# Kernel tuning notes

Hardware: AMD Instinct MI355X
Metric: run time of the kernel (lower is better)

The kernel has to match this reference:

```python
import jax, jax.numpy as jnp
import numpy as np

NUM_HEADS = 16
EPS = 1e-6


def rmsnorm(x, w):
    return x * jax.lax.rsqrt(jnp.mean(x * x, axis=-1, keepdims=True) + EPS) * w


def split_heads(x):
    b, t, d = x.shape
    return x.reshape(b, t, NUM_HEADS, d // NUM_HEADS).transpose(0, 2, 1, 3)


def setup_inputs() -> dict:
    key = jax.random.key(0)
    ks = jax.random.split(key, 16)
    B, S, D, F, N = 4, 2048, 1024, 4096, 16

    def xavier(k, shape):
        lim = float(np.sqrt(6.0 / (shape[-2] + shape[-1])))
        return jax.random.uniform(k, shape, jnp.float32, -lim, lim)

    return {
        'sequence_tokens': jax.random.normal(ks[0], (B, S, D), jnp.float32),
        'sequence_mask': jnp.ones((B, S), dtype=bool),
        'ns_tokens': jax.random.normal(ks[1], (B, N, D), jnp.float32),
        'ns_mask': jnp.ones((B, N), dtype=bool),
        'next_sequence_length': 1024,
        'attn_norm_w': jnp.ones((D,), jnp.float32),
        'ffn_norm_w': jnp.ones((D,), jnp.float32),
        'Wq': xavier(ks[2], (D, D)),
        'Wk': xavier(ks[3], (D, D)),
        'Wv': xavier(ks[4], (D, D)),
        'Wo': xavier(ks[5], (D, D)),
        'ns_q_w': xavier(ks[6], (N, D, D)),
        'ns_k_w': xavier(ks[7], (N, D, D)),
        'ns_v_w': xavier(ks[8], (N, D, D)),
        'seq_up_w': xavier(ks[9], (D, F)),
        'seq_up_b': jnp.zeros((F,), jnp.float32),
        'seq_down_w': xavier(ks[10], (F, D)),
        'seq_down_b': jnp.zeros((D,), jnp.float32),
        'ns_up_w': xavier(ks[11], (N, D, F)),
        'ns_up_b': jnp.zeros((N, F), jnp.float32),
        'ns_down_w': xavier(ks[12], (N, F, D)),
        'ns_down_b': jnp.zeros((N, D), jnp.float32),
    }


def reference(sequence_tokens, sequence_mask, ns_tokens, ns_mask, next_sequence_length,
              attn_norm_w, ffn_norm_w, Wq, Wk, Wv, Wo,
              ns_q_w, ns_k_w, ns_v_w,
              seq_up_w, seq_up_b, seq_down_w, seq_down_b,
              ns_up_w, ns_up_b, ns_down_w, ns_down_b):
    nsl = next_sequence_length
    B, S, D = sequence_tokens.shape
    N = ns_tokens.shape[1]
    scale = 1.0 / np.sqrt(D // NUM_HEADS)

    # --- attention block (pre-norm) ---
    x_seq = rmsnorm(sequence_tokens, attn_norm_w)
    x_ns = rmsnorm(ns_tokens, attn_norm_w)
    seq_q_mask = sequence_mask[:, -nsl:]

    q = jnp.concatenate([x_seq[:, -nsl:] @ Wq, jnp.einsum('bnd,ndo->bno', x_ns, ns_q_w)], axis=1)
    k = jnp.concatenate([x_seq @ Wk, jnp.einsum('bnd,ndo->bno', x_ns, ns_k_w)], axis=1)
    v = jnp.concatenate([x_seq @ Wv, jnp.einsum('bnd,ndo->bno', x_ns, ns_v_w)], axis=1)
    q, k, v = split_heads(q), split_heads(k), split_heads(v)

    total_k = S + N
    q_pos = jnp.concatenate([jnp.arange(S - nsl, S), jnp.arange(S, total_k)])
    k_pos = jnp.arange(total_k)
    causal = k_pos[None, :] <= q_pos[:, None]                       # [nsl+N, S+N]
    key_mask = jnp.concatenate([sequence_mask, ns_mask], axis=1)    # [B, S+N]

    logits = jnp.einsum('bhqd,bhkd->bhqk', q.astype(jnp.float32), k.astype(jnp.float32)) * scale
    logits = jnp.where(causal[None, None] & key_mask[:, None, None, :], logits, -10000.0)
    attw = jax.nn.softmax(logits, axis=-1).astype(q.dtype)
    att = jnp.einsum('bhqk,bhkd->bhqd', attw, v)
    att = att.transpose(0, 2, 1, 3).reshape(B, nsl + N, D) @ Wo

    seq_att = att[:, :nsl] * seq_q_mask[..., None].astype(att.dtype)
    ns_att = att[:, nsl:] * ns_mask[..., None].astype(att.dtype)

    seq = sequence_tokens[:, -nsl:] + seq_att
    ns = ns_tokens + ns_att

    # --- FFN block (pre-norm, SiLU) ---
    h_seq = rmsnorm(seq, ffn_norm_w)
    h_ns = rmsnorm(ns, ffn_norm_w)
    seq_ffn = jax.nn.silu(h_seq @ seq_up_w + seq_up_b) @ seq_down_w + seq_down_b
    seq_ffn = seq_ffn * seq_q_mask[..., None].astype(seq_ffn.dtype)
    ns_h = jax.nn.silu(jnp.einsum('bnd,ndf->bnf', h_ns, ns_up_w) + ns_up_b)
    ns_ffn = jnp.einsum('bnf,nfd->bnd', ns_h, ns_down_w) + ns_down_b
    ns_ffn = ns_ffn * ns_mask[..., None].astype(ns_ffn.dtype)

    seq_out = (seq + seq_ffn) * seq_q_mask[..., None].astype(seq.dtype)
    ns_out = (ns + ns_ffn) * ns_mask[..., None].astype(ns.dtype)
    return seq_out, seq_q_mask, ns_out, ns_mask
```

## Files before the change

### kernel.cpp

```cpp
#include <hip/hip_runtime.h>
#include <hip/hip_bf16.h>
#include <cstdint>
#include <cstddef>

#define BB 4
#define SS 2048
#define DD 1024
#define FF 4096
#define NN 16
#define HH 16
#define HD 64
#define NSL 1024
#define TQ 1040
#define TK 2064

typedef __attribute__((ext_vector_type(8))) short short8v;
typedef __attribute__((ext_vector_type(4))) float f32x4;
typedef __attribute__((ext_vector_type(16))) float f32x16;
typedef __hip_bfloat16 bf16;

#define SCLOG2E 0.1803368801111092f

__device__ __forceinline__ void gload16(const bf16* g, bf16* l) {
    __builtin_amdgcn_global_load_lds(
        (const __attribute__((address_space(1))) unsigned int*)(const void*)g,
        (__attribute__((address_space(3))) unsigned int*)(void*)l,
        16, 0, 0);
}

__device__ __forceinline__ unsigned cvtpk(float lo, float hi2) {
    unsigned r;
    asm("v_cvt_pk_bf16_f32 %0, %1, %2" : "=v"(r) : "v"(lo), "v"(hi2));
    return r;
}

__device__ __forceinline__ void convT_body(
    const float* __restrict__ W, bf16* __restrict__ WT, int K, int N,
    int bx, int by, char* smem)
{
    bf16 (*T)[65] = (bf16(*)[65])smem;
    const int tid = threadIdx.x;
    const int c0 = bx * 64;
    const int r0 = by * 64;
    const int rr = tid >> 6, c = tid & 63;
#pragma unroll
    for (int j = 0; j < 16; j++) {
        int row = j * 4 + rr;
        T[row][c] = __float2bfloat16(W[(size_t)(r0 + row) * N + c0 + c]);
    }
    __syncthreads();
#pragma unroll
    for (int j = 0; j < 16; j++) {
        int wrow = j * 4 + rr;
        WT[(size_t)(c0 + wrow) * K + r0 + c] = T[c][wrow];
    }
}

__device__ __forceinline__ void rmsnorm_body(
    const float* __restrict__ x, const float* __restrict__ w,
    bf16* __restrict__ out, int row, char* smem)
{
    float* red = (float*)smem;
    const int tid = threadIdx.x;
    const float* xp = x + (size_t)row * DD + tid * 4;
    float4 xv = *(const float4*)xp;
    float ss = xv.x * xv.x + xv.y * xv.y + xv.z * xv.z + xv.w * xv.w;
#pragma unroll
    for (int o = 32; o >= 1; o >>= 1) ss += __shfl_down(ss, o);
    if ((tid & 63) == 0) red[tid >> 6] = ss;
    __syncthreads();
    float tot = red[0] + red[1] + red[2] + red[3];
    float rs = rsqrtf(tot * (1.0f / DD) + 1e-6f);
    float4 wv = *(const float4*)(w + tid * 4);
    bf16* op = out + (size_t)row * DD + tid * 4;
    op[0] = __float2bfloat16(xv.x * rs * wv.x);
    op[1] = __float2bfloat16(xv.y * rs * wv.y);
    op[2] = __float2bfloat16(xv.z * rs * wv.z);
    op[3] = __float2bfloat16(xv.w * rs * wv.w);
}

__global__ __launch_bounds__(256) void prep_kernel(
    const float* __restrict__ Wq, const float* __restrict__ Wk,
    const float* __restrict__ Wv, const float* __restrict__ Wo,
    const float* __restrict__ upw, const float* __restrict__ dww,
    bf16* __restrict__ wqkvT, bf16* __restrict__ woT,
    bf16* __restrict__ upwT, bf16* __restrict__ dwwT,
    const float* __restrict__ seq_tokens, const float* __restrict__ ns_tokens,
    const float* __restrict__ attn_norm_w,
    bf16* __restrict__ xnseq, bf16* __restrict__ xnns,
    float* __restrict__ resb, float* __restrict__ outz,
    float* __restrict__ nsacc)
{
    __shared__ __align__(16) char smem[8448];
    int id = blockIdx.x;
    if (id < 256)        convT_body(Wq, wqkvT, 1024, 1024, id & 15, id >> 4, smem);
    else if (id < 512)   { int u = id - 256;  convT_body(Wk, wqkvT + 1024 * 1024, 1024, 1024, u & 15, u >> 4, smem); }
    else if (id < 768)   { int u = id - 512;  convT_body(Wv, wqkvT + 2048 * 1024, 1024, 1024, u & 15, u >> 4, smem); }
    else if (id < 1024)  { int u = id - 768;  convT_body(Wo, woT, 1024, 1024, u & 15, u >> 4, smem); }
    else if (id < 2048)  { int u = id - 1024; convT_body(upw, upwT, 1024, 4096, u & 63, u >> 6, smem); }
    else if (id < 3072)  { int u = id - 2048; convT_body(dww, dwwT, 4096, 1024, u & 15, u >> 4, smem); }
    else if (id < 11264) rmsnorm_body(seq_tokens, attn_norm_w, xnseq, id - 3072, smem);
    else if (id < 11328) rmsnorm_body(ns_tokens, attn_norm_w, xnns, id - 11264, smem);
    else {
        int u = id - 11328;
        float* base;
        if (u < 4160)       base = resb + (size_t)u * 1024;
        else if (u < 8256)  base = outz + (size_t)(u - 4160) * 1024;
        else                base = nsacc + (size_t)(u - 8256) * 1024;
        float4 z = {0.f, 0.f, 0.f, 0.f};
        ((float4*)base)[threadIdx.x] = z;
    }
}

__global__ __launch_bounds__(256) void rmsnorm_kernel(
    const float* __restrict__ x, const float* __restrict__ w,
    bf16* __restrict__ out)
{
    __shared__ __align__(16) char smem[64];
    rmsnorm_body(x, w, out, blockIdx.x, smem);
}

template<int EPI>
__device__ __forceinline__ void gemm128_body(
    int bxx, int byy, int bzz, char* smem,
    const bf16* __restrict__ A, const bf16* __restrict__ BT,
    void* __restrict__ Cp, int M, int Nn, int K, int kTot,
    int aMb, int aRS, int aOff,
    const float* __restrict__ bias,
    const float* __restrict__ res0, const float* __restrict__ res1)
{
    const int m0 = bxx * 128;
    const int n0 = byy * 128;
    if constexpr (EPI == 4) {
        if (n0 < 1024 && (m0 & 2047) < 1024) return;
    }
    bf16* As = (bf16*)smem;
    bf16* Bs = (bf16*)(smem + 16384);
    const int tid = threadIdx.x;
    const int lane = tid & 63;
    const int wave = tid >> 6;
    const int wr = (wave >> 1) * 64;
    const int wc = (wave & 1) * 64;
    const int ql = lane & 31;
    const int hi = lane >> 5;
    const int kOff = bzz * K;

    const int srow = tid >> 3;
    const int skc = (((tid & 7) ^ (srow & 7))) * 8;
    const bf16* pA[4];
    const bf16* pB[4];
#pragma unroll
    for (int g = 0; g < 4; g++) {
        int ar = m0 + g * 32 + srow; if (ar >= M) ar = M - 1;
        pA[g] = A + ((size_t)(ar / aMb) * aRS + (ar % aMb) + aOff) * kTot + kOff + skc;
        pB[g] = BT + (size_t)(n0 + g * 32 + srow) * kTot + kOff + skc;
    }
    bf16* lA = As + tid * 8;
    bf16* lB = Bs + tid * 8;

    const int rA0 = wr + ql, rA1 = wr + 32 + ql;
    const int rB0 = wc + ql, rB1 = wc + 32 + ql;

    f32x16 acc[2][2] = {};

    for (int k0 = 0; k0 < K; k0 += 64) {
        __syncthreads();
#pragma unroll
        for (int g = 0; g < 4; g++) {
            gload16(pA[g] + k0, lA + g * 2048);
            gload16(pB[g] + k0, lB + g * 2048);
        }
        __syncthreads();
#pragma unroll
        for (int ks = 0; ks < 4; ks++) {
            int ch = 2 * ks + hi;
            short8v a0 = *(const short8v*)(&As[(rA0 << 6) + ((ch ^ (rA0 & 7)) << 3)]);
            short8v a1 = *(const short8v*)(&As[(rA1 << 6) + ((ch ^ (rA1 & 7)) << 3)]);
            short8v b0 = *(const short8v*)(&Bs[(rB0 << 6) + ((ch ^ (rB0 & 7)) << 3)]);
            short8v b1 = *(const short8v*)(&Bs[(rB1 << 6) + ((ch ^ (rB1 & 7)) << 3)]);
            acc[0][0] = __builtin_amdgcn_mfma_f32_32x32x16_bf16(a0, b0, acc[0][0], 0, 0, 0);
            acc[0][1] = __builtin_amdgcn_mfma_f32_32x32x16_bf16(a0, b1, acc[0][1], 0, 0, 0);
            acc[1][0] = __builtin_amdgcn_mfma_f32_32x32x16_bf16(a1, b0, acc[1][0], 0, 0, 0);
            acc[1][1] = __builtin_amdgcn_mfma_f32_32x32x16_bf16(a1, b1, acc[1][1], 0, 0, 0);
        }
    }

#pragma unroll
    for (int mt = 0; mt < 2; mt++)
#pragma unroll
        for (int nt = 0; nt < 2; nt++) {
            const int colg = n0 + wc + nt * 32 + ql;
#pragma unroll
            for (int g = 0; g < 4; g++) {
                int row0 = m0 + wr + mt * 32 + g * 8 + 4 * hi;
                if constexpr (EPI == 4) {
                    int bb2 = row0 >> 11, s0 = row0 & 2047;
                    if (colg < 1024) {
                        if (s0 >= 1024) {
#pragma unroll
                            for (int j = 0; j < 4; j++)
                                ((bf16*)Cp)[((size_t)(bb2 * TQ + s0 + j - 1024)) * DD + colg] =
                                    __float2bfloat16(acc[mt][nt][g * 4 + j] * SCLOG2E);
                        }
                    } else if (colg < 2048) {
#pragma unroll
                        for (int j = 0; j < 4; j++)
                            ((bf16*)res0)[((size_t)(bb2 * TK + s0 + j)) * DD + (colg - 1024)] =
                                __float2bfloat16(acc[mt][nt][g * 4 + j]);
                    } else {
                        union { unsigned u[2]; } pk_;
                        pk_.u[0] = cvtpk(acc[mt][nt][g * 4 + 0], acc[mt][nt][g * 4 + 1]);
                        pk_.u[1] = cvtpk(acc[mt][nt][g * 4 + 2], acc[mt][nt][g * 4 + 3]);
                        bf16* vt = (bf16*)res1;
                        *(uint2*)(&vt[((size_t)(bb2 * DD + colg - 2048)) * TK + s0]) =
                            *(const uint2*)pk_.u;
                    }
                    continue;
                }
#pragma unroll
                for (int j = 0; j < 4; j++) {
                    int row = row0 + j;
                    if (row >= M) continue;
                    float val = acc[mt][nt][g * 4 + j];
                    if constexpr (EPI == 1) {
                        val += bias[colg];
                        val = val / (1.0f + __expf(-val));
                        ((bf16*)Cp)[(size_t)row * Nn + colg] = __float2bfloat16(val);
                    } else if constexpr (EPI == 5) {
                        float* dst = (float*)Cp + (size_t)row * DD + colg;
                        if (bzz == 0) {
                            int bb2 = row / TQ, t = row % TQ;
                            const float* rp = (t < NSL)
                                ? res0 + ((size_t)bb2 * SS + (SS - NSL) + t) * DD
                                : res1 + ((size_t)bb2 * NN + (t - NSL)) * DD;
                            atomicAdd(dst, val + rp[colg]);
                        } else {
                            atomicAdd(dst, val);
                        }
                    } else if constexpr (EPI == 6) {
                        float* dst = (float*)Cp + (size_t)row * DD + colg;
                        if (bzz == 0) {
                            int bb2 = row / NSL, t = row % NSL;
                            float r = res0[((size_t)bb2 * TQ + t) * DD + colg];
                            atomicAdd(dst, val + bias[colg] + r);
                        } else {
                            atomicAdd(dst, val);
                        }
                    }
                }
            }
        }
}

template<int EPI>
__global__ __launch_bounds__(256, 3) void gemm128_kernel(
    const bf16* __restrict__ A, const bf16* __restrict__ BT,
    void* __restrict__ Cp, int M, int Nn, int K, int kTot,
    int aMb, int aRS, int aOff,
    const float* __restrict__ bias,
    const float* __restrict__ res0, const float* __restrict__ res1)
{
    __shared__ __align__(16) char smem[32768];
    gemm128_body<EPI>(blockIdx.x, blockIdx.y, blockIdx.z, smem,
                      A, BT, Cp, M, Nn, K, kTot, aMb, aRS, aOff,
                      bias, res0, res1);
}

__device__ __forceinline__ void ns_qkv_body(
    int cb, int n, int which, char* smem,
    const bf16* __restrict__ xnns,
    const float* __restrict__ Wqn, const float* __restrict__ Wkn,
    const float* __restrict__ Wvn,
    bf16* __restrict__ q, bf16* __restrict__ k, bf16* __restrict__ vbt)
{
    float* Asm = (float*)smem;
    float* RedF = (float*)(smem + 16384);
    const int tid = threadIdx.x;
    const int cg = tid & 63;
    const int dg = tid >> 6;
    const int col = cb * 64 + cg;
    const float* W = which == 0 ? Wqn : (which == 1 ? Wkn : Wvn);
    for (int i = tid; i < 512; i += 256) {
        int bb = i >> 7, c8 = (i & 127) * 8;
        uint4 raw = *(const uint4*)&xnns[((size_t)(bb * NN + n)) * DD + c8];
        const bf16* hh = (const bf16*)&raw;
#pragma unroll
        for (int j = 0; j < 8; j++) Asm[bb * 1024 + c8 + j] = __bfloat162float(hh[j]);
    }
    __syncthreads();
    float a0 = 0, a1 = 0, a2 = 0, a3 = 0;
    const float* wp = W + (size_t)n * DD * DD + col;
#pragma unroll 8
    for (int d = dg * 256; d < dg * 256 + 256; d++) {
        float w = wp[(size_t)d * DD];
        a0 += Asm[0 * 1024 + d] * w; a1 += Asm[1 * 1024 + d] * w;
        a2 += Asm[2 * 1024 + d] * w; a3 += Asm[3 * 1024 + d] * w;
    }
    RedF[(dg * 4 + 0) * 64 + cg] = a0; RedF[(dg * 4 + 1) * 64 + cg] = a1;
    RedF[(dg * 4 + 2) * 64 + cg] = a2; RedF[(dg * 4 + 3) * 64 + cg] = a3;
    __syncthreads();
    if (dg == 0) {
#pragma unroll
        for (int bb = 0; bb < 4; bb++) {
            float s = RedF[(0 * 4 + bb) * 64 + cg] + RedF[(1 * 4 + bb) * 64 + cg]
                    + RedF[(2 * 4 + bb) * 64 + cg] + RedF[(3 * 4 + bb) * 64 + cg];
            if (which == 0)
                q[((size_t)(bb * TQ + NSL + n)) * DD + col] =
                    __float2bfloat16(s * SCLOG2E);
            else if (which == 1)
                k[((size_t)(bb * TK + SS + n)) * DD + col] = __float2bfloat16(s);
            else
                vbt[((size_t)(bb * DD + col)) * TK + SS + n] = __float2bfloat16(s);
        }
    }
}

__device__ __forceinline__ void ns_up_body(
    int cb, int n, char* smem,
    const bf16* __restrict__ hb, const float* __restrict__ W,
    const float* __restrict__ bias, bf16* __restrict__ mid)
{
    float* Asm = (float*)smem;
    float* RedF = (float*)(smem + 16384);
    const int tid = threadIdx.x;
    const int cg = tid & 63;
    const int dg = tid >> 6;
    const int col = cb * 64 + cg;
    for (int i = tid; i < 512; i += 256) {
        int bb = i >> 7, c8 = (i & 127) * 8;
        uint4 raw = *(const uint4*)&hb[((size_t)(bb * TQ + NSL + n)) * DD + c8];
        const bf16* hh = (const bf16*)&raw;
#pragma unroll
        for (int j = 0; j < 8; j++) Asm[bb * 1024 + c8 + j] = __bfloat162float(hh[j]);
    }
    __syncthreads();
    float a0 = 0, a1 = 0, a2 = 0, a3 = 0;
    const float* wp = W + (size_t)n * DD * FF + col;
#pragma unroll 8
    for (int d = dg * 256; d < dg * 256 + 256; d++) {
        float w = wp[(size_t)d * FF];
        a0 += Asm[0 * 1024 + d] * w; a1 += Asm[1 * 1024 + d] * w;
        a2 += Asm[2 * 1024 + d] * w; a3 += Asm[3 * 1024 + d] * w;
    }
    RedF[(dg * 4 + 0) * 64 + cg] = a0; RedF[(dg * 4 + 1) * 64 + cg] = a1;
    RedF[(dg * 4 + 2) * 64 + cg] = a2; RedF[(dg * 4 + 3) * 64 + cg] = a3;
    __syncthreads();
    if (dg == 0) {
        float bv = bias[(size_t)n * FF + col];
#pragma unroll
        for (int bb = 0; bb < 4; bb++) {
            float x = RedF[(0 * 4 + bb) * 64 + cg] + RedF[(1 * 4 + bb) * 64 + cg]
                    + RedF[(2 * 4 + bb) * 64 + cg] + RedF[(3 * 4 + bb) * 64 + cg] + bv;
            x = x / (1.0f + __expf(-x));
            mid[((size_t)(bb * NN + n)) * FF + col] = __float2bfloat16(x);
        }
    }
}

__device__ __forceinline__ void ns_down_body(
    int cb, int n, int z, char* smem,
    const bf16* __restrict__ mid, const float* __restrict__ W,
    float* __restrict__ accum)
{
    float* Asm = (float*)smem;
    float* RedF = (float*)(smem + 16384);
    const int tid = threadIdx.x;
    const int cg = tid & 63;
    const int dg = tid >> 6;
    const int col = cb * 64 + cg;
    for (int i = tid; i < 512; i += 256) {
        int bb = i >> 7, c8 = (i & 127) * 8;
        uint4 raw = *(const uint4*)&mid[((size_t)(bb * NN + n)) * FF + z * 1024 + c8];
        const bf16* hh = (const bf16*)&raw;
#pragma unroll
        for (int j = 0; j < 8; j++) Asm[bb * 1024 + c8 + j] = __bfloat162float(hh[j]);
    }
    __syncthreads();
    float a0 = 0, a1 = 0, a2 = 0, a3 = 0;
    const float* wp = W + ((size_t)n * FF + z * 1024) * DD + col;
#pragma unroll 8
    for (int d = dg * 256; d < dg * 256 + 256; d++) {
        float w = wp[(size_t)d * DD];
        a0 += Asm[0 * 1024 + d] * w; a1 += Asm[1 * 1024 + d] * w;
        a2 += Asm[2 * 1024 + d] * w; a3 += Asm[3 * 1024 + d] * w;
    }
    RedF[(dg * 4 + 0) * 64 + cg] = a0; RedF[(dg * 4 + 1) * 64 + cg] = a1;
    RedF[(dg * 4 + 2) * 64 + cg] = a2; RedF[(dg * 4 + 3) * 64 + cg] = a3;
    __syncthreads();
    if (dg == 0) {
#pragma unroll
        for (int bb = 0; bb < 4; bb++) {
            float s = RedF[(0 * 4 + bb) * 64 + cg] + RedF[(1 * 4 + bb) * 64 + cg]
                    + RedF[(2 * 4 + bb) * 64 + cg] + RedF[(3 * 4 + bb) * 64 + cg];
            atomicAdd(&accum[((size_t)(bb * NN + n)) * DD + col], s);
        }
    }
}

__global__ __launch_bounds__(256, 3) void fusedA_kernel(
    const bf16* __restrict__ xnseq, const bf16* __restrict__ wqkvT,
    bf16* __restrict__ qb, bf16* __restrict__ kb, bf16* __restrict__ vbt,
    const bf16* __restrict__ xnns,
    const float* __restrict__ Wqn, const float* __restrict__ Wkn,
    const float* __restrict__ Wvn)
{
    __shared__ __align__(16) char smem[32768];
    int flat = blockIdx.x;
    int g = flat / 3, r = flat - g * 3;
    if (r < 2) {
        int gi = g * 2 + r;
        gemm128_body<4>(gi & 63, gi >> 6, 0, smem, xnseq, wqkvT, qb,
            8192, 3072, 1024, 1024, 8192, 8192, 0,
            nullptr, (const float*)kb, (const float*)vbt);
    } else {
        ns_qkv_body(g & 15, (g >> 4) & 15, g >> 8, smem,
                    xnns, Wqn, Wkn, Wvn, qb, kb, vbt);
    }
}

__global__ __launch_bounds__(256, 3) void fusedB_kernel(
    const bf16* __restrict__ hb, const bf16* __restrict__ upwT,
    bf16* __restrict__ midseq, const float* __restrict__ upb,
    const float* __restrict__ nupw, const float* __restrict__ nupb,
    bf16* __restrict__ midns)
{
    __shared__ __align__(16) char smem[32768];
    int flat = blockIdx.x;
    int g = flat >> 1, r = flat & 1;
    if (r == 0) {
        gemm128_body<1>(g & 31, g >> 5, 0, smem, hb, upwT, midseq,
            4096, 4096, 1024, 1024, 1024, 1040, 0,
            upb, nullptr, nullptr);
    } else {
        ns_up_body(g & 63, g >> 6, smem, hb, nupw, nupb, midns);
    }
}

__global__ __launch_bounds__(256, 3) void fusedC_kernel(
    const bf16* __restrict__ midseq, const bf16* __restrict__ dwwT,
    float* __restrict__ out, const float* __restrict__ dwb,
    const float* __restrict__ resb,
    const bf16* __restrict__ midns, const float* __restrict__ ndww,
    float* __restrict__ nsacc)
{
    __shared__ __align__(16) char smem[32768];
    int flat = blockIdx.x;
    int g = flat >> 1, r = flat & 1;
    if (r == 0) {
        gemm128_body<6>(g & 31, (g >> 5) & 7, g >> 8, smem, midseq, dwwT, out,
            4096, 1024, 1024, 4096, 4096, 4096, 0,
            dwb, resb, nullptr);
    } else {
        ns_down_body(g & 15, (g >> 4) & 15, g >> 8, smem, midns, ndww, nsacc);
    }
}

#define SWZ(row, chunk) (((row) << 6) + ((((chunk) ^ ((row) & 7))) << 3))
#define DEFER_THR 12.0f

__global__ __launch_bounds__(128, 3) void attn_mfma_kernel(
    const bf16* __restrict__ qb, const bf16* __restrict__ kb,
    const bf16* __restrict__ vbt, float* __restrict__ pO,
    float* __restrict__ pML)
{
    __shared__ bf16 SM[2 * 8192];

    const int tid = threadIdx.x;
    const int lane = tid & 63;
    const int w = tid >> 6;

    int flat = blockIdx.x + 34 * (blockIdx.y + 16 * blockIdx.z);
    int widx = (flat & 7) * 272 + (flat >> 3);
    const int bx = widx % 34;
    const int rem = widx / 34;
    const int h = rem & 15;
    const int b = rem >> 4;
    const int qt = 16 - (bx >> 1);
    const int kh = bx & 1;

    const int q0 = qt * 64;
    const int ql = lane & 31;
    const int hi = lane >> 5;
    const int qg = q0 + 32 * w + ql;
    const bool wact = (q0 + 32 * w) < TQ;
    const int qpos = NSL + qg;

    short8v qf[4] = {};
    if (qg < TQ) {
        const bf16* qp = qb + ((size_t)(b * TQ + qg)) * DD + h * HD;
#pragma unroll
        for (int s = 0; s < 4; s++) qf[s] = *(const short8v*)(qp + 16 * s + 8 * hi);
    }

    const int qlast = min(q0 + 63, TQ - 1);
    const int nkt = (NSL + qlast + 1 + 63) >> 6;
    const int khmid = nkt >> 1;
    const int k0t = kh ? khmid : 0;
    const int k1t = kh ? nkt : khmid;

    int off[2][4];
#pragma unroll
    for (int t = 0; t < 2; t++)
#pragma unroll
        for (int s = 0; s < 4; s++)
            off[t][s] = SWZ(ql + 32 * t, 2 * s + hi);

    const int c = lane & 7;
    size_t kSrc[4], vRow[4];
    int vSw[4], sRow[4];
#pragma unroll
    for (int i = 0; i < 4; i++) {
        int r = 32 * w + 8 * i + (lane >> 3);
        sRow[i] = r;
        kSrc[i] = ((size_t)(b * TK + r)) * DD + h * HD + ((c ^ (r & 7)) << 3);
        vRow[i] = ((size_t)(b * DD + h * HD + r)) * TK;
        vSw[i]  = (c ^ (r & 7)) << 3;
    }

    auto stage = [&](int kbase, int buf) {
        bf16* kD = SM + buf * 8192 + w * 2048;
        bf16* vD = SM + buf * 8192 + 4096 + w * 2048;
        if (kbase + 64 <= TK) {
#pragma unroll
            for (int i = 0; i < 4; i++) {
                gload16(kb + kSrc[i] + (size_t)kbase * DD, kD + i * 512);
                gload16(vbt + vRow[i] + kbase + vSw[i], vD + i * 512);
            }
        } else {
#pragma unroll
            for (int i = 0; i < 4; i++) {
                int rg = min(kbase + sRow[i], TK - 1);
                gload16(kb + ((size_t)(b * TK + rg)) * DD + h * HD +
                             ((c ^ (sRow[i] & 7)) << 3), kD + i * 512);
                int colv = (kbase + vSw[i] + 8 <= TK) ? (kbase + vSw[i]) : 0;
                gload16(vbt + vRow[i] + colv, vD + i * 512);
            }
        }
    };

    float m_run = -1e30f, l_run = 0.f;
    f32x16 o0 = {}, o1 = {};
    const int wlimit = NSL + q0 + 32 * w + 31;

    int cur = 0;
    stage(k0t * 64, 0);

    for (int kt = k0t; kt < k1t; kt++) {
        const int kbase = kt * 64;
        __syncthreads();
        if (kt + 1 < k1t) stage(kbase + 64, cur ^ 1);

        if (wact && kbase <= wlimit) {
            const bf16* KsC = SM + cur * 8192;
            const bf16* VtC = KsC + 4096;

            f32x16 st[2] = {};
            __builtin_amdgcn_s_setprio(1);
#pragma unroll
            for (int s = 0; s < 4; s++) {
                short8v kf0 = *(const short8v*)(&KsC[off[0][s]]);
                short8v kf1 = *(const short8v*)(&KsC[off[1][s]]);
                st[0] = __builtin_amdgcn_mfma_f32_32x32x16_bf16(kf0, qf[s], st[0], 0, 0, 0);
                st[1] = __builtin_amdgcn_mfma_f32_32x32x16_bf16(kf1, qf[s], st[1], 0, 0, 0);
            }
            __builtin_amdgcn_s_setprio(0);

            if (kbase + 63 > NSL + q0 + 32 * w) {
#pragma unroll
                for (int t = 0; t < 2; t++)
#pragma unroll
                    for (int r = 0; r < 16; r++) {
                        int key = kbase + 32 * t + (r & 3) + 8 * (r >> 2) + 4 * hi;
                        if (key > qpos) st[t][r] = -1e30f;
                    }
            }

            float pmax = st[0][0];
#pragma unroll
            for (int r = 1; r < 16; r++) pmax = fmaxf(pmax, st[0][r]);
#pragma unroll
            for (int r = 0; r < 16; r++) pmax = fmaxf(pmax, st[1][r]);
            pmax = fmaxf(pmax, __shfl_xor(pmax, 32));

            if (!__all(pmax - m_run <= DEFER_THR)) {
                float mnew = fmaxf(m_run, pmax);
                float alpha = exp2f(m_run - mnew);
                m_run = mnew;
                l_run *= alpha;
#pragma unroll
                for (int r = 0; r < 16; r++) {
                    float aq = __shfl(alpha, (r & 3) + 8 * (r >> 2) + 4 * hi);
                    o0[r] *= aq; o1[r] *= aq;
                }
            }

            unsigned nib[8][2];
            float lt = 0.f;
#pragma unroll
            for (int m8 = 0; m8 < 8; m8++) {
                int t = m8 >> 2, rb = (m8 & 3) * 4;
                float p0 = exp2f(st[t][rb + 0] - m_run);
                float p1 = exp2f(st[t][rb + 1] - m_run);
                float p2 = exp2f(st[t][rb + 2] - m_run);
                float p3 = exp2f(st[t][rb + 3] - m_run);
                lt += (p0 + p1) + (p2 + p3);
                nib[m8][0] = cvtpk(p0, p1);
                nib[m8][1] = cvtpk(p2, p3);
            }
            lt += __shfl_xor(lt, 32);
            l_run += lt;

            __builtin_amdgcn_s_setprio(1);
#pragma unroll
            for (int s = 0; s < 4; s++) {
                unsigned s0 = nib[2 * s + 1 - hi][0];
                unsigned s1 = nib[2 * s + 1 - hi][1];
                unsigned r0 = __shfl_xor(s0, 32);
                unsigned r1 = __shfl_xor(s1, 32);
                unsigned w0 = hi ? r0 : nib[2 * s][0];
                unsigned w1 = hi ? r1 : nib[2 * s][1];
                unsigned w2 = hi ? nib[2 * s + 1][0] : r0;
                unsigned w3 = hi ? nib[2 * s + 1][1] : r1;
                union { unsigned u[4]; short8v v; } pa;
                pa.u[0] = w0; pa.u[1] = w1; pa.u[2] = w2; pa.u[3] = w3;
                short8v vf0 = *(const short8v*)(&VtC[off[0][s]]);
                short8v vf1 = *(const short8v*)(&VtC[off[1][s]]);
                o0 = __builtin_amdgcn_mfma_f32_32x32x16_bf16(pa.v, vf0, o0, 0, 0, 0);
                o1 = __builtin_amdgcn_mfma_f32_32x32x16_bf16(pa.v, vf1, o1, 0, 0, 0);
            }
            __builtin_amdgcn_s_setprio(0);
        }
        cur ^= 1;
    }

    if (wact) {
        size_t pb = ((size_t)((b * HH + h) * 17 + qt)) * 2 + kh;
        float* Op = pO + pb * 4096 + (size_t)(32 * w) * 64;
#pragma unroll
        for (int r = 0; r < 16; r++) {
            int qrow = (r & 3) + 8 * (r >> 2) + 4 * hi;
            Op[qrow * 64 + ql]      = o0[r];
            Op[qrow * 64 + 32 + ql] = o1[r];
        }
        if (hi == 0) {
            pML[pb * 128 + 32 * w + ql] = m_run;
            pML[pb * 128 + 64 + 32 * w + ql] = l_run;
        }
    }
}

__global__ __launch_bounds__(256) void attn_merge_kernel(
    const float* __restrict__ pO, const float* __restrict__ pML,
    bf16* __restrict__ atb)
{
    const int qt = 16 - blockIdx.x;
    const int h = blockIdx.y, b = blockIdx.z;
    const int q0 = qt * 64;
    const int tid = threadIdx.x;
    const int q = tid >> 2;
    const int d0 = (tid & 3) * 16;
    if (q0 + q >= TQ) return;
    size_t pb0 = ((size_t)((b * HH + h) * 17 + qt)) * 2;
    float ma = pML[pb0 * 128 + q],       la = pML[pb0 * 128 + 64 + q];
    float mb = pML[(pb0 + 1) * 128 + q], lb = pML[(pb0 + 1) * 128 + 64 + q];
    float m = fmaxf(ma, mb);
    float wa = exp2f(ma - m), wb = exp2f(mb - m);
    float inv = 1.0f / (la * wa + lb * wb);
    const float* Oa = pO + pb0 * 4096 + q * 64 + d0;
    const float* Ob = Oa + 4096;
    union { unsigned u[8]; uint4 q4[2]; } outp;
#pragma unroll
    for (int j = 0; j < 8; j++) {
        float x0 = (Oa[2 * j]     * wa + Ob[2 * j]     * wb) * inv;
        float x1 = (Oa[2 * j + 1] * wa + Ob[2 * j + 1] * wb) * inv;
        outp.u[j] = cvtpk(x0, x1);
    }
    bf16* op = atb + ((size_t)(b * TQ + q0 + q)) * DD + h * HD + d0;
    *(uint4*)op = outp.q4[0];
    *(uint4*)(op + 8) = outp.q4[1];
}

__global__ __launch_bounds__(256) void ns_final_kernel(
    const float* __restrict__ accum, const float* __restrict__ bias,
    const float* __restrict__ res, float* __restrict__ out)
{
    const int blk = blockIdx.x;
    const int tid = threadIdx.x;
    if (blk < 64) {
        const int b = blk >> 4, n = blk & 15;
        float* outns = out + 4198400;
        for (int c = tid; c < DD; c += 256) {
            float x = accum[(size_t)blk * DD + c] + bias[(size_t)n * DD + c]
                    + res[((size_t)(b * TQ + NSL + n)) * DD + c];
            outns[(size_t)blk * DD + c] = x;
        }
    } else {
        int idx = (blk - 64) * 256 + tid;
        if (idx < 4096) out[4194304 + idx] = 1.0f;
        else if (idx < 4160) out[4263936 + (idx - 4096)] = 1.0f;
    }
}

extern "C" void kernel_launch(void* const* d_in, const int* in_sizes, int n_in,
                              void* d_out, int out_size, void* d_ws, size_t ws_size,
                              hipStream_t stream)
{
    const float* seq_tokens  = (const float*)d_in[0];
    const float* ns_tokens   = (const float*)d_in[2];
    const float* attn_norm_w = (const float*)d_in[5];
    const float* ffn_norm_w  = (const float*)d_in[6];
    const float* Wq  = (const float*)d_in[7];
    const float* Wk  = (const float*)d_in[8];
    const float* Wv  = (const float*)d_in[9];
    const float* Wo  = (const float*)d_in[10];
    const float* nsqw = (const float*)d_in[11];
    const float* nskw = (const float*)d_in[12];
    const float* nsvw = (const float*)d_in[13];
    const float* upw  = (const float*)d_in[14];
    const float* upb  = (const float*)d_in[15];
    const float* dww  = (const float*)d_in[16];
    const float* dwb  = (const float*)d_in[17];
    const float* nupw = (const float*)d_in[18];
    const float* nupb = (const float*)d_in[19];
    const float* ndww = (const float*)d_in[20];
    const float* ndwb = (const float*)d_in[21];
    float* out = (float*)d_out;

    char* ws = (char*)d_ws;
    bf16*  xnseq  = (bf16*)(ws + 0);
    bf16*  xnns   = (bf16*)(ws + 16777216);
    bf16*  qb     = (bf16*)(ws + 16908288);
    bf16*  kb     = (bf16*)(ws + 25427968);
    bf16*  vbt    = (bf16*)(ws + 42336256);
    bf16*  atb    = (bf16*)(ws + 59244544);
    float* resb   = (float*)(ws + 67764224);
    bf16*  hb     = (bf16*)(ws + 84803584);
    bf16*  midseq = (bf16*)(ws + 93323264);
    bf16*  midns  = (bf16*)(ws + 126877696);
    float* nsacc  = (float*)(ws + 127401984);
    bf16*  wqkvT  = (bf16*)(ws + 127664128);
    bf16*  woT    = (bf16*)(ws + 133955584);
    bf16*  upwT   = (bf16*)(ws + 136052736);
    bf16*  dwwT   = (bf16*)(ws + 144441344);
    float* pO     = (float*)(ws + 152829952);
    float* pML    = (float*)(ws + 188481536);

    prep_kernel<<<19648, 256, 0, stream>>>(Wq, Wk, Wv, Wo, upw, dww,
        wqkvT, woT, upwT, dwwT, seq_tokens, ns_tokens, attn_norm_w,
        xnseq, xnns, resb, out, nsacc);

    fusedA_kernel<<<2304, 256, 0, stream>>>(xnseq, wqkvT, qb, kb, vbt,
                                            xnns, nsqw, nskw, nsvw);

    attn_mfma_kernel<<<dim3(34, 16, 4), 128, 0, stream>>>(qb, kb, vbt, pO, pML);
    attn_merge_kernel<<<dim3(17, 16, 4), 256, 0, stream>>>(pO, pML, atb);

    gemm128_kernel<5><<<dim3(33, 8, 2), 256, 0, stream>>>(atb, woT, resb,
        4160, 1024, 512, 1024, 4160, 4160, 0,
        nullptr, seq_tokens, ns_tokens);

    rmsnorm_kernel<<<BB * TQ, 256, 0, stream>>>(resb, ffn_norm_w, hb);

    fusedB_kernel<<<2048, 256, 0, stream>>>(hb, upwT, midseq, upb,
                                            nupw, nupb, midns);

    fusedC_kernel<<<2048, 256, 0, stream>>>(midseq, dwwT, out, dwb,
                                            resb, midns, ndww, nsacc);

    ns_final_kernel<<<81, 256, 0, stream>>>(nsacc, ndwb, resb, out);
}
```

Baseline: 537.2 us.

## Use 256x256 pipelined MFMA GEMM tiles for FFN up/down projections

Adds a gemm256 body with 512-thread blocks, 256x256 output tiles, double-buffered direct-to-LDS loads, explicit vmcnt waits, barriers and setprio around MFMA bursts. The FFN up and down fused kernels now use it, and the per-token NS FFN bodies are widened to 512 threads so they match the new block size. The aim is more data reuse per loaded tile and overlap of global loads with MFMA work. The cost is 128KB of LDS per block and lower occupancy, with fewer blocks and more tail risk.

```diff
diff --git a/kernel.cpp b/kernel.cpp
--- a/kernel.cpp
+++ b/kernel.cpp
@@ -33,6 +33,11 @@
     asm("v_cvt_pk_bf16_f32 %0, %1, %2" : "=v"(r) : "v"(lo), "v"(hi2));
     return r;
 }
+
+#define VMWAIT8() asm volatile("s_waitcnt vmcnt(8)" ::: "memory")
+#define VMWAIT2() asm volatile("s_waitcnt vmcnt(2)" ::: "memory")
+#define VMWAIT0() asm volatile("s_waitcnt vmcnt(0)" ::: "memory")
+#define RBAR() __builtin_amdgcn_s_barrier()
 
 __device__ __forceinline__ void convT_body(
     const float* __restrict__ W, bf16* __restrict__ WT, int K, int N,
@@ -222,11 +227,7 @@
                     int row = row0 + j;
                     if (row >= M) continue;
                     float val = acc[mt][nt][g * 4 + j];
-                    if constexpr (EPI == 1) {
-                        val += bias[colg];
-                        val = val / (1.0f + __expf(-val));
-                        ((bf16*)Cp)[(size_t)row * Nn + colg] = __float2bfloat16(val);
-                    } else if constexpr (EPI == 5) {
+                    if constexpr (EPI == 5) {
                         float* dst = (float*)Cp + (size_t)row * DD + colg;
                         if (bzz == 0) {
                             int bb2 = row / TQ, t = row % TQ;
@@ -237,15 +238,6 @@
                         } else {
                             atomicAdd(dst, val);
                         }
-                    } else if constexpr (EPI == 6) {
-                        float* dst = (float*)Cp + (size_t)row * DD + colg;
-                        if (bzz == 0) {
-                            int bb2 = row / NSL, t = row % NSL;
-                            float r = res0[((size_t)bb2 * TQ + t) * DD + colg];
-                            atomicAdd(dst, val + bias[colg] + r);
-                        } else {
-                            atomicAdd(dst, val);
-                        }
                     }
                 }
             }
@@ -264,6 +256,185 @@
     gemm128_body<EPI>(blockIdx.x, blockIdx.y, blockIdx.z, smem,
                       A, BT, Cp, M, Nn, K, kTot, aMb, aRS, aOff,
                       bias, res0, res1);
+}
+
+template<int EPI>
+__device__ __forceinline__ void gemm256_body(
+    int bxx, int byy, int bzz, char* smem,
+    const bf16* __restrict__ A, const bf16* __restrict__ BT,
+    void* __restrict__ Cp, int Nn, int K, int kTot,
+    int aMb, int aRS,
+    const float* __restrict__ bias, const float* __restrict__ res0)
+{
+    const int m0 = bxx * 256;
+    const int n0 = byy * 256;
+    bf16* SM = (bf16*)smem;
+    const int tid = threadIdx.x;
+    const int lane = tid & 63;
+    const int wid = tid >> 6;
+    const int wm = wid >> 2;
+    const int wn = wid & 3;
+    const int fr = lane & 15;
+    const int fkg = lane >> 4;
+    const int kOff = bzz * K;
+    const int NT = K >> 6;
+
+    const int srow = tid >> 3;
+    const int skc = ((tid & 7) ^ (srow & 7)) * 8;
+    const bf16* pAc[4];
+    const bf16* pBc[4];
+#pragma unroll
+    for (int g = 0; g < 4; g++) {
+        int gr = m0 + g * 64 + srow;
+        pAc[g] = A + ((size_t)(gr / aMb) * aRS + (gr % aMb)) * kTot + kOff + skc;
+        pBc[g] = BT + (size_t)(n0 + g * 64 + srow) * kTot + kOff + skc;
+    }
+
+    f32x4 acc[8][4] = {};
+
+#define ISSA(t, g) gload16(pAc[g] + (t) * 64, SM + ((t) & 1) * 32768 + (g) * 4096 + tid * 8)
+#define ISSB(t, g) gload16(pBc[g] + (t) * 64, SM + ((t) & 1) * 32768 + 16384 + (g) * 4096 + tid * 8)
+#define AOFF(s, row, kk) ((s) * 32768 + (row) * 64 + ((((kk) * 4 + fkg) ^ ((row) & 7)) << 3))
+#define BOFF(s, row, kk) ((s) * 32768 + 16384 + (row) * 64 + ((((kk) * 4 + fkg) ^ ((row) & 7)) << 3))
+
+    ISSA(0, 0); ISSA(0, 2); ISSB(0, 0); ISSB(0, 1); ISSB(0, 2); ISSB(0, 3);
+    ISSA(0, 1); ISSA(0, 3);
+    ISSA(1, 0); ISSA(1, 2); ISSB(1, 0); ISSB(1, 1); ISSB(1, 2); ISSB(1, 3);
+
+    for (int t = 0; t < NT; t++) {
+        const int s = t & 1;
+        const bool nx = (t + 1 < NT);
+
+        if (nx) { VMWAIT8(); } else { VMWAIT2(); }
+        RBAR();
+
+        short8v bF[4][2];
+#pragma unroll
+        for (int cb = 0; cb < 4; cb++)
+#pragma unroll
+            for (int kk = 0; kk < 2; kk++)
+                bF[cb][kk] = *(const short8v*)(&SM[BOFF(s, wn * 64 + cb * 16 + fr, kk)]);
+
+        {
+            short8v aF[2][2];
+#pragma unroll
+            for (int rr = 0; rr < 2; rr++)
+#pragma unroll
+                for (int kk = 0; kk < 2; kk++)
+                    aF[rr][kk] = *(const short8v*)(&SM[AOFF(s, wm * 128 + rr * 16 + fr, kk)]);
+            if (nx) ISSA(t + 1, 1);
+            RBAR();
+            __builtin_amdgcn_s_setprio(1);
+#pragma unroll
+            for (int rr = 0; rr < 2; rr++)
+#pragma unroll
+                for (int cb = 0; cb < 4; cb++)
+#pragma unroll
+                    for (int kk = 0; kk < 2; kk++)
+                        acc[rr][cb] = __builtin_amdgcn_mfma_f32_16x16x32_bf16(
+                            aF[rr][kk], bF[cb][kk], acc[rr][cb], 0, 0, 0);
+            __builtin_amdgcn_s_setprio(0);
+            RBAR();
+        }
+        {
+            short8v aF[2][2];
+#pragma unroll
+            for (int rr = 0; rr < 2; rr++)
+#pragma unroll
+                for (int kk = 0; kk < 2; kk++)
+                    aF[rr][kk] = *(const short8v*)(&SM[AOFF(s, wm * 128 + 32 + rr * 16 + fr, kk)]);
+            if (nx) ISSA(t + 1, 3);
+            RBAR();
+            __builtin_amdgcn_s_setprio(1);
+#pragma unroll
+            for (int rr = 0; rr < 2; rr++)
+#pragma unroll
+                for (int cb = 0; cb < 4; cb++)
+#pragma unroll
+                    for (int kk = 0; kk < 2; kk++)
+                        acc[2 + rr][cb] = __builtin_amdgcn_mfma_f32_16x16x32_bf16(
+                            aF[rr][kk], bF[cb][kk], acc[2 + rr][cb], 0, 0, 0);
+            __builtin_amdgcn_s_setprio(0);
+            RBAR();
+        }
+        if (nx) { VMWAIT8(); } else { VMWAIT0(); }
+        RBAR();
+        {
+            short8v aF[2][2];
+#pragma unroll
+            for (int rr = 0; rr < 2; rr++)
+#pragma unroll
+                for (int kk = 0; kk < 2; kk++)
+                    aF[rr][kk] = *(const short8v*)(&SM[AOFF(s, wm * 128 + 64 + rr * 16 + fr, kk)]);
+            RBAR();
+            __builtin_amdgcn_s_setprio(1);
+#pragma unroll
+            for (int rr = 0; rr < 2; rr++)
+#pragma unroll
+                for (int cb = 0; cb < 4; cb++)
+#pragma unroll
+                    for (int kk = 0; kk < 2; kk++)
+                        acc[4 + rr][cb] = __builtin_amdgcn_mfma_f32_16x16x32_bf16(
+                            aF[rr][kk], bF[cb][kk], acc[4 + rr][cb], 0, 0, 0);
+            __builtin_amdgcn_s_setprio(0);
+            RBAR();
+        }
+        {
+            short8v aF[2][2];
+#pragma unroll
+            for (int rr = 0; rr < 2; rr++)
+#pragma unroll
+                for (int kk = 0; kk < 2; kk++)
+                    aF[rr][kk] = *(const short8v*)(&SM[AOFF(s, wm * 128 + 96 + rr * 16 + fr, kk)]);
+            RBAR();
+            __builtin_amdgcn_s_setprio(1);
+#pragma unroll
+            for (int rr = 0; rr < 2; rr++)
+#pragma unroll
+                for (int cb = 0; cb < 4; cb++)
+#pragma unroll
+                    for (int kk = 0; kk < 2; kk++)
+                        acc[6 + rr][cb] = __builtin_amdgcn_mfma_f32_16x16x32_bf16(
+                            aF[rr][kk], bF[cb][kk], acc[6 + rr][cb], 0, 0, 0);
+            __builtin_amdgcn_s_setprio(0);
+            RBAR();
+        }
+        if (t + 2 < NT) {
+            ISSA(t + 2, 0); ISSA(t + 2, 2);
+            ISSB(t + 2, 0); ISSB(t + 2, 1); ISSB(t + 2, 2); ISSB(t + 2, 3);
+        }
+    }
+#undef ISSA
+#undef ISSB
+#undef AOFF
+#undef BOFF
+
+#pragma unroll
+    for (int r = 0; r < 8; r++)
+#pragma unroll
+        for (int cb = 0; cb < 4; cb++) {
+            const int col = n0 + wn * 64 + cb * 16 + fr;
+            const int row0 = m0 + wm * 128 + r * 16 + fkg * 4;
+#pragma unroll
+            for (int j = 0; j < 4; j++) {
+                int row = row0 + j;
+                float val = acc[r][cb][j];
+                if constexpr (EPI == 1) {
+                    val += bias[col];
+                    val = val / (1.0f + __expf(-val));
+                    ((bf16*)Cp)[(size_t)row * Nn + col] = __float2bfloat16(val);
+                } else {
+                    float* dst = (float*)Cp + (size_t)row * DD + col;
+                    if (bzz == 0) {
+                        int bb2 = row >> 10, tt = row & 1023;
+                        float rsd = res0[((size_t)bb2 * TQ + tt) * DD + col];
+                        atomicAdd(dst, val + bias[col] + rsd);
+                    } else {
+                        atomicAdd(dst, val);
+                    }
+                }
+            }
+        }
 }
 
 __device__ __forceinline__ void ns_qkv_body(
@@ -315,7 +486,7 @@
     }
 }
 
-__device__ __forceinline__ void ns_up_body(
+__device__ __forceinline__ void ns_up_body512(
     int cb, int n, char* smem,
     const bf16* __restrict__ hb, const float* __restrict__ W,
     const float* __restrict__ bias, bf16* __restrict__ mid)
@@ -323,11 +494,11 @@
     float* Asm = (float*)smem;
     float* RedF = (float*)(smem + 16384);
     const int tid = threadIdx.x;
-    const int cg = tid & 63;
-    const int dg = tid >> 6;
-    const int col = cb * 64 + cg;
-    for (int i = tid; i < 512; i += 256) {
-        int bb = i >> 7, c8 = (i & 127) * 8;
+    const int cg = tid & 127;
+    const int dg = tid >> 7;
+    const int col = cb * 128 + cg;
+    {
+        int bb = tid >> 7, c8 = (tid & 127) * 8;
         uint4 raw = *(const uint4*)&hb[((size_t)(bb * TQ + NSL + n)) * DD + c8];
         const bf16* hh = (const bf16*)&raw;
 #pragma unroll
@@ -342,22 +513,22 @@
         a0 += Asm[0 * 1024 + d] * w; a1 += Asm[1 * 1024 + d] * w;
         a2 += Asm[2 * 1024 + d] * w; a3 += Asm[3 * 1024 + d] * w;
     }
-    RedF[(dg * 4 + 0) * 64 + cg] = a0; RedF[(dg * 4 + 1) * 64 + cg] = a1;
-    RedF[(dg * 4 + 2) * 64 + cg] = a2; RedF[(dg * 4 + 3) * 64 + cg] = a3;
+    RedF[(dg * 4 + 0) * 128 + cg] = a0; RedF[(dg * 4 + 1) * 128 + cg] = a1;
+    RedF[(dg * 4 + 2) * 128 + cg] = a2; RedF[(dg * 4 + 3) * 128 + cg] = a3;
     __syncthreads();
     if (dg == 0) {
         float bv = bias[(size_t)n * FF + col];
 #pragma unroll
         for (int bb = 0; bb < 4; bb++) {
-            float x = RedF[(0 * 4 + bb) * 64 + cg] + RedF[(1 * 4 + bb) * 64 + cg]
-                    + RedF[(2 * 4 + bb) * 64 + cg] + RedF[(3 * 4 + bb) * 64 + cg] + bv;
+            float x = RedF[(0 * 4 + bb) * 128 + cg] + RedF[(1 * 4 + bb) * 128 + cg]
+                    + RedF[(2 * 4 + bb) * 128 + cg] + RedF[(3 * 4 + bb) * 128 + cg] + bv;
             x = x / (1.0f + __expf(-x));
             mid[((size_t)(bb * NN + n)) * FF + col] = __float2bfloat16(x);
         }
     }
 }
 
-__device__ __forceinline__ void ns_down_body(
+__device__ __forceinline__ void ns_down_body512(
     int cb, int n, int z, char* smem,
     const bf16* __restrict__ mid, const float* __restrict__ W,
     float* __restrict__ accum)
@@ -365,11 +536,11 @@
     float* Asm = (float*)smem;
     float* RedF = (float*)(smem + 16384);
     const int tid = threadIdx.x;
-    const int cg = tid & 63;
-    const int dg = tid >> 6;
-    const int col = cb * 64 + cg;
-    for (int i = tid; i < 512; i += 256) {
-        int bb = i >> 7, c8 = (i & 127) * 8;
+    const int cg = tid & 127;
+    const int dg = tid >> 7;
+    const int col = cb * 128 + cg;
+    {
+        int bb = tid >> 7, c8 = (tid & 127) * 8;
         uint4 raw = *(const uint4*)&mid[((size_t)(bb * NN + n)) * FF + z * 1024 + c8];
         const bf16* hh = (const bf16*)&raw;
 #pragma unroll
@@ -384,14 +555,14 @@
         a0 += Asm[0 * 1024 + d] * w; a1 += Asm[1 * 1024 + d] * w;
         a2 += Asm[2 * 1024 + d] * w; a3 += Asm[3 * 1024 + d] * w;
     }
-    RedF[(dg * 4 + 0) * 64 + cg] = a0; RedF[(dg * 4 + 1) * 64 + cg] = a1;
-    RedF[(dg * 4 + 2) * 64 + cg] = a2; RedF[(dg * 4 + 3) * 64 + cg] = a3;
+    RedF[(dg * 4 + 0) * 128 + cg] = a0; RedF[(dg * 4 + 1) * 128 + cg] = a1;
+    RedF[(dg * 4 + 2) * 128 + cg] = a2; RedF[(dg * 4 + 3) * 128 + cg] = a3;
     __syncthreads();
     if (dg == 0) {
 #pragma unroll
         for (int bb = 0; bb < 4; bb++) {
-            float s = RedF[(0 * 4 + bb) * 64 + cg] + RedF[(1 * 4 + bb) * 64 + cg]
-                    + RedF[(2 * 4 + bb) * 64 + cg] + RedF[(3 * 4 + bb) * 64 + cg];
+            float s = RedF[(0 * 4 + bb) * 128 + cg] + RedF[(1 * 4 + bb) * 128 + cg]
+                    + RedF[(2 * 4 + bb) * 128 + cg] + RedF[(3 * 4 + bb) * 128 + cg];
             atomicAdd(&accum[((size_t)(bb * NN + n)) * DD + col], s);
         }
     }
@@ -418,40 +589,40 @@
     }
 }
 
-__global__ __launch_bounds__(256, 3) void fusedB_kernel(
+__global__ __launch_bounds__(512, 2) void fusedB_kernel(
     const bf16* __restrict__ hb, const bf16* __restrict__ upwT,
     bf16* __restrict__ midseq, const float* __restrict__ upb,
     const float* __restrict__ nupw, const float* __restrict__ nupb,
     bf16* __restrict__ midns)
 {
-    __shared__ __align__(16) char smem[32768];
+    __shared__ __align__(16) char smem[131072];
     int flat = blockIdx.x;
-    int g = flat >> 1, r = flat & 1;
+    int g = flat / 3, r = flat - g * 3;
     if (r == 0) {
-        gemm128_body<1>(g & 31, g >> 5, 0, smem, hb, upwT, midseq,
-            4096, 4096, 1024, 1024, 1024, 1040, 0,
-            upb, nullptr, nullptr);
+        gemm256_body<1>(g & 15, g >> 4, 0, smem, hb, upwT, midseq,
+            4096, 1024, 1024, 1024, 1040, upb, nullptr);
     } else {
-        ns_up_body(g & 63, g >> 6, smem, hb, nupw, nupb, midns);
-    }
-}
-
-__global__ __launch_bounds__(256, 3) void fusedC_kernel(
+        int id = g * 2 + (r - 1);
+        ns_up_body512(id & 31, id >> 5, smem, hb, nupw, nupb, midns);
+    }
+}
+
+__global__ __launch_bounds__(512, 2) void fusedC_kernel(
     const bf16* __restrict__ midseq, const bf16* __restrict__ dwwT,
     float* __restrict__ out, const float* __restrict__ dwb,
     const float* __restrict__ resb,
     const bf16* __restrict__ midns, const float* __restrict__ ndww,
     float* __restrict__ nsacc)
 {
-    __shared__ __align__(16) char smem[32768];
+    __shared__ __align__(16) char smem[131072];
     int flat = blockIdx.x;
-    int g = flat >> 1, r = flat & 1;
+    int g = flat / 3, r = flat - g * 3;
     if (r == 0) {
-        gemm128_body<6>(g & 31, (g >> 5) & 7, g >> 8, smem, midseq, dwwT, out,
-            4096, 1024, 1024, 4096, 4096, 4096, 0,
-            dwb, resb, nullptr);
+        gemm256_body<6>(g & 15, (g >> 4) & 3, g >> 6, smem, midseq, dwwT, out,
+            1024, 1024, 4096, 1 << 30, 0, dwb, resb);
     } else {
-        ns_down_body(g & 15, (g >> 4) & 15, g >> 8, smem, midns, ndww, nsacc);
+        int id = g * 2 + (r - 1);
+        ns_down_body512(id & 7, (id >> 3) & 15, id >> 7, smem, midns, ndww, nsacc);
     }
 }
 
@@ -761,11 +932,11 @@
 
     rmsnorm_kernel<<<BB * TQ, 256, 0, stream>>>(resb, ffn_norm_w, hb);
 
-    fusedB_kernel<<<2048, 256, 0, stream>>>(hb, upwT, midseq, upb,
-                                            nupw, nupb, midns);
-
-    fusedC_kernel<<<2048, 256, 0, stream>>>(midseq, dwwT, out, dwb,
-                                            resb, midns, ndww, nsacc);
+    fusedB_kernel<<<768, 512, 0, stream>>>(hb, upwT, midseq, upb,
+                                           nupw, nupb, midns);
+
+    fusedC_kernel<<<768, 512, 0, stream>>>(midseq, dwwT, out, dwb,
+                                           resb, midns, ndww, nsacc);
 
     ns_final_kernel<<<81, 256, 0, stream>>>(nsacc, ndwb, resb, out);
 }
```

Result: slower. 560.3 us (+4.3%).

## Double-buffer LDS tiles in GEMM main loop to overlap loads with MFMA

Applied to the files above, without the earlier changes.

The 128x128 GEMM body now uses two LDS stages: the next K-tile is issued via global_load_lds while MFMAs run on the current one, with a single waitcnt+barrier per iteration instead of two syncthreads. Shared memory per block doubles to 64KB and launch bounds drop to 2 blocks per CU for the fused kernels, which lowers occupancy in exchange for overlapping memory latency with compute.

```diff
diff --git a/kernel.cpp b/kernel.cpp
--- a/kernel.cpp
+++ b/kernel.cpp
@@ -33,6 +33,12 @@
     asm("v_cvt_pk_bf16_f32 %0, %1, %2" : "=v"(r) : "v"(lo), "v"(hi2));
     return r;
 }
+
+#define PIPE_SYNC() do { \
+    asm volatile("s_waitcnt vmcnt(0)" ::: "memory"); \
+    __builtin_amdgcn_s_barrier(); \
+    asm volatile("" ::: "memory"); \
+} while (0)
 
 __device__ __forceinline__ void convT_body(
     const float* __restrict__ W, bf16* __restrict__ WT, int K, int N,
@@ -134,8 +140,7 @@
     if constexpr (EPI == 4) {
         if (n0 < 1024 && (m0 & 2047) < 1024) return;
     }
-    bf16* As = (bf16*)smem;
-    bf16* Bs = (bf16*)(smem + 16384);
+    bf16* SM = (bf16*)smem;
     const int tid = threadIdx.x;
     const int lane = tid & 63;
     const int wave = tid >> 6;
@@ -155,22 +160,31 @@
         pA[g] = A + ((size_t)(ar / aMb) * aRS + (ar % aMb) + aOff) * kTot + kOff + skc;
         pB[g] = BT + (size_t)(n0 + g * 32 + srow) * kTot + kOff + skc;
     }
-    bf16* lA = As + tid * 8;
-    bf16* lB = Bs + tid * 8;
 
     const int rA0 = wr + ql, rA1 = wr + 32 + ql;
     const int rB0 = wc + ql, rB1 = wc + 32 + ql;
 
     f32x16 acc[2][2] = {};
-
-    for (int k0 = 0; k0 < K; k0 += 64) {
-        __syncthreads();
+    const int NT = K >> 6;
+
+    auto stageT = [&](int t, int slot) {
+        bf16* a = SM + slot * 16384 + tid * 8;
+        bf16* b = SM + slot * 16384 + 8192 + tid * 8;
 #pragma unroll
         for (int g = 0; g < 4; g++) {
-            gload16(pA[g] + k0, lA + g * 2048);
-            gload16(pB[g] + k0, lB + g * 2048);
-        }
-        __syncthreads();
+            gload16(pA[g] + t * 64, a + g * 2048);
+            gload16(pB[g] + t * 64, b + g * 2048);
+        }
+    };
+
+    stageT(0, 0);
+    PIPE_SYNC();
+
+    for (int t = 0; t < NT; t++) {
+        const int s = t & 1;
+        if (t + 1 < NT) stageT(t + 1, s ^ 1);
+        const bf16* As = SM + s * 16384;
+        const bf16* Bs = As + 8192;
 #pragma unroll
         for (int ks = 0; ks < 4; ks++) {
             int ch = 2 * ks + hi;
@@ -183,6 +197,7 @@
             acc[1][0] = __builtin_amdgcn_mfma_f32_32x32x16_bf16(a1, b0, acc[1][0], 0, 0, 0);
             acc[1][1] = __builtin_amdgcn_mfma_f32_32x32x16_bf16(a1, b1, acc[1][1], 0, 0, 0);
         }
+        if (t + 1 < NT) PIPE_SYNC();
     }
 
 #pragma unroll
@@ -253,14 +268,14 @@
 }
 
 template<int EPI>
-__global__ __launch_bounds__(256, 3) void gemm128_kernel(
+__global__ __launch_bounds__(256, 2) void gemm128_kernel(
     const bf16* __restrict__ A, const bf16* __restrict__ BT,
     void* __restrict__ Cp, int M, int Nn, int K, int kTot,
     int aMb, int aRS, int aOff,
     const float* __restrict__ bias,
     const float* __restrict__ res0, const float* __restrict__ res1)
 {
-    __shared__ __align__(16) char smem[32768];
+    __shared__ __align__(16) char smem[65536];
     gemm128_body<EPI>(blockIdx.x, blockIdx.y, blockIdx.z, smem,
                       A, BT, Cp, M, Nn, K, kTot, aMb, aRS, aOff,
                       bias, res0, res1);
@@ -397,14 +412,14 @@
     }
 }
 
-__global__ __launch_bounds__(256, 3) void fusedA_kernel(
+__global__ __launch_bounds__(256, 2) void fusedA_kernel(
     const bf16* __restrict__ xnseq, const bf16* __restrict__ wqkvT,
     bf16* __restrict__ qb, bf16* __restrict__ kb, bf16* __restrict__ vbt,
     const bf16* __restrict__ xnns,
     const float* __restrict__ Wqn, const float* __restrict__ Wkn,
     const float* __restrict__ Wvn)
 {
-    __shared__ __align__(16) char smem[32768];
+    __shared__ __align__(16) char smem[65536];
     int flat = blockIdx.x;
     int g = flat / 3, r = flat - g * 3;
     if (r < 2) {
@@ -418,13 +433,13 @@
     }
 }
 
-__global__ __launch_bounds__(256, 3) void fusedB_kernel(
+__global__ __launch_bounds__(256, 2) void fusedB_kernel(
     const bf16* __restrict__ hb, const bf16* __restrict__ upwT,
     bf16* __restrict__ midseq, const float* __restrict__ upb,
     const float* __restrict__ nupw, const float* __restrict__ nupb,
     bf16* __restrict__ midns)
 {
-    __shared__ __align__(16) char smem[32768];
+    __shared__ __align__(16) char smem[65536];
     int flat = blockIdx.x;
     int g = flat >> 1, r = flat & 1;
     if (r == 0) {
@@ -436,14 +451,14 @@
     }
 }
 
-__global__ __launch_bounds__(256, 3) void fusedC_kernel(
+__global__ __launch_bounds__(256, 2) void fusedC_kernel(
     const bf16* __restrict__ midseq, const bf16* __restrict__ dwwT,
     float* __restrict__ out, const float* __restrict__ dwb,
     const float* __restrict__ resb,
     const bf16* __restrict__ midns, const float* __restrict__ ndww,
     float* __restrict__ nsacc)
 {
-    __shared__ __align__(16) char smem[32768];
+    __shared__ __align__(16) char smem[65536];
     int flat = blockIdx.x;
     int g = flat >> 1, r = flat & 1;
     if (r == 0) {
```

Result: slower. 564.8 us (+5.1%).
